# Performance work log

Hardware: AMD Instinct MI355X
Metric: run time of the kernel (lower is better)

The kernel has to match this reference:

```python
import jax, jax.numpy as jnp
import numpy as np

N_NODES = 50000
N_EDGES = 400000
N_GRAPHS = 250
D = 256
NUM_FEATURES = 256
NUM_CLASSES = 10
N_EXTRA_LAYERS = 4  # num_layers - 1
BN_EPS = 1e-5


def _mean_agg(x, src, dst, n):
    # DGL copy_u + mean over incoming edges; zero in-degree nodes get 0.
    s = jax.ops.segment_sum(x[src], dst, num_segments=n)           # [N, d]
    deg = jax.ops.segment_sum(jnp.ones((src.shape[0],), x.dtype), dst, num_segments=n)
    deg = deg[:, None]
    return jnp.where(deg > 0, s / jnp.maximum(deg, 1.0), 0.0)


def _gin_layer(x, src, dst, W1, b1, W2, b2, gamma, beta):
    n = x.shape[0]
    h = x + _mean_agg(x, src, dst, n)                              # (1+eps)*x + agg, eps=0
    h = jax.nn.relu(h @ W1 + b1) @ W2 + b2                         # apply_func MLP
    h = jax.nn.relu(h)                                             # GINConv activation
    mu = h.mean(axis=0)
    var = h.var(axis=0)                                            # biased var (torch BN train)
    return gamma * (h - mu) / jnp.sqrt(var + BN_EPS) + beta


def setup_inputs() -> dict:
    key = jax.random.key(0)
    ks = jax.random.split(key, 24)
    sc_in = 1.0 / np.sqrt(NUM_FEATURES)
    sc = 1.0 / np.sqrt(D)
    inp = {
        "x": jax.random.normal(ks[0], (N_NODES, NUM_FEATURES), dtype=jnp.float32),
        "src": jax.random.randint(ks[1], (N_EDGES,), 0, N_NODES, dtype=jnp.int32),
        "dst": jax.random.randint(ks[2], (N_EDGES,), 0, N_NODES, dtype=jnp.int32),
        "node_counts": jnp.full((N_GRAPHS,), N_NODES // N_GRAPHS, dtype=jnp.int32),
        # conv1 MLP + BN1
        "W1a": jax.random.normal(ks[3], (NUM_FEATURES, D), dtype=jnp.float32) * sc_in,
        "b1a": jnp.zeros((D,), jnp.float32),
        "W1b": jax.random.normal(ks[4], (D, D), dtype=jnp.float32) * sc,
        "b1b": jnp.zeros((D,), jnp.float32),
        "g1": jnp.ones((D,), jnp.float32),
        "be1": jnp.zeros((D,), jnp.float32),
        # stacked convs 2..5 + BNs
        "Ws1": jax.random.normal(ks[5], (N_EXTRA_LAYERS, D, D), dtype=jnp.float32) * sc,
        "bs1": jnp.zeros((N_EXTRA_LAYERS, D), jnp.float32),
        "Ws2": jax.random.normal(ks[6], (N_EXTRA_LAYERS, D, D), dtype=jnp.float32) * sc,
        "bs2": jnp.zeros((N_EXTRA_LAYERS, D), jnp.float32),
        "gammas": jnp.ones((N_EXTRA_LAYERS, D), jnp.float32),
        "betas": jnp.zeros((N_EXTRA_LAYERS, D), jnp.float32),
        # classifier
        "fcW1": jax.random.normal(ks[7], (D, D), dtype=jnp.float32) * sc,
        "fcb1": jnp.zeros((D,), jnp.float32),
        "fcW2": jax.random.normal(ks[8], (D, NUM_CLASSES), dtype=jnp.float32) * sc,
        "fcb2": jnp.zeros((NUM_CLASSES,), jnp.float32),
    }
    return inp


def reference(x, src, dst, node_counts, W1a, b1a, W1b, b1b, g1, be1,
              Ws1, bs1, Ws2, bs2, gammas, betas, fcW1, fcb1, fcW2, fcb2):
    h = _gin_layer(x, src, dst, W1a, b1a, W1b, b1b, g1, be1)
    for i in range(N_EXTRA_LAYERS):
        h = _gin_layer(h, src, dst, Ws1[i], bs1[i], Ws2[i], bs2[i], gammas[i], betas[i])
    # per-graph last-node readout
    last_idx = jnp.cumsum(node_counts) - 1                          # [n_graphs]
    g = h[last_idx]                                                 # [n_graphs, d]
    # dropout is identity in eval mode
    g = jax.nn.relu(g @ fcW1 + fcb1)
    logits = g @ fcW2 + fcb2
    return jax.nn.log_softmax(logits, axis=-1)
```

## Files before the change

kernel.cpp:

```cpp
#include <hip/hip_runtime.h>
#include <hip/hip_bf16.h>

#define N_NODESC 50000
#define N_EDGESC 400000
#define N_GRAPHSC 250
#define DDIM 256
#define NCLS 10
#define BN_EPSF 1e-5f
#define MPAD 50048
#define NBLK_GEMM 391
#define NBLK_SCAN 196

typedef __attribute__((ext_vector_type(4))) float f32x4;
typedef __attribute__((ext_vector_type(8))) short bf16x8;
typedef __attribute__((ext_vector_type(8))) unsigned short u16x8;

__device__ __forceinline__ float bf2f(unsigned short h) {
    union { unsigned int u; float f; } c;
    c.u = ((unsigned int)h) << 16;
    return c.f;
}
__device__ __forceinline__ unsigned short f2bf(float f) {
    union { float f; unsigned int u; } c;
    c.f = f;
    unsigned int u = c.u;
    return (unsigned short)((u + 0x7FFFu + ((u >> 16) & 1u)) >> 16);
}

__device__ __forceinline__ void gld_lds16(const void* g, void* l) {
    __builtin_amdgcn_global_load_lds(
        (const __attribute__((address_space(1))) unsigned int*)g,
        (__attribute__((address_space(3))) unsigned int*)l, 16, 0, 0);
}


__global__ void k_zero32(int* __restrict__ p, int n) {
    int i = blockIdx.x * blockDim.x + threadIdx.x;
    if (i < n) p[i] = 0;
}

__global__ void k_count(const int* __restrict__ dst, int* __restrict__ cnt) {
    int e = blockIdx.x * blockDim.x + threadIdx.x;
    if (e < N_EDGESC) atomicAdd(&cnt[dst[e]], 1);
}

__global__ __launch_bounds__(256) void k_scan1(const int* __restrict__ deg,
                                               int* __restrict__ rowstart,
                                               int* __restrict__ bsum) {
    __shared__ int sh[256];
    int tid = threadIdx.x;
    int i = blockIdx.x * 256 + tid;
    int v = (i < N_NODESC) ? deg[i] : 0;
    sh[tid] = v;
    __syncthreads();
    for (int off = 1; off < 256; off <<= 1) {
        int t = (tid >= off) ? sh[tid - off] : 0;
        __syncthreads();
        sh[tid] += t;
        __syncthreads();
    }
    if (i < N_NODESC) rowstart[i] = sh[tid] - v;
    if (tid == 255) bsum[blockIdx.x] = sh[255];
}

__global__ __launch_bounds__(256) void k_scan2(int* __restrict__ rowstart,
                                               const int* __restrict__ bsum) {
    __shared__ int sh[256];
    int tid = threadIdx.x;
    sh[tid] = (tid < NBLK_SCAN) ? bsum[tid] : 0;
    __syncthreads();
    for (int off = 1; off < 256; off <<= 1) {
        int t = (tid >= off) ? sh[tid - off] : 0;
        __syncthreads();
        sh[tid] += t;
        __syncthreads();
    }
    int i = blockIdx.x * 256 + tid;
    if (blockIdx.x > 0 && i < N_NODESC) rowstart[i] += sh[blockIdx.x - 1];
    if (i == 0) rowstart[N_NODESC] = N_EDGESC;
}

__global__ void k_fill(const int* __restrict__ src, const int* __restrict__ dst,
                       const int* __restrict__ rowstart, int* __restrict__ cur,
                       int* __restrict__ esrc) {
    int e = blockIdx.x * blockDim.x + threadIdx.x;
    if (e < N_EDGESC) {
        int d = dst[e];
        int pos = rowstart[d] + atomicAdd(&cur[d], 1);
        esrc[pos] = src[e];
    }
}


__global__ __launch_bounds__(256) void k_wprep(const float* __restrict__ W1a,
                                               const float* __restrict__ W1b,
                                               const float* __restrict__ Ws1,
                                               const float* __restrict__ Ws2,
                                               unsigned short* __restrict__ Wt) {
    int i = blockIdx.x * blockDim.x + threadIdx.x;
    if (i >= 10 * 65536) return;
    int m = i >> 16;
    int r = i & 65535;
    int n = r >> 8;
    int k = r & 255;
    int l = m >> 1, wsel = m & 1;
    const float* src = (l == 0) ? (wsel ? W1b : W1a)
                                : (wsel ? Ws2 + (size_t)(l - 1) * 65536
                                        : Ws1 + (size_t)(l - 1) * 65536);
    Wt[i] = f2bf(src[(size_t)k * 256 + n]);
}

__global__ __launch_bounds__(256) void k_xbf(const float* __restrict__ X,
                                             unsigned short* __restrict__ Y) {
    int i = blockIdx.x * 256 + threadIdx.x;
    if (i < N_NODESC * 64) {
        float4 v = ((const float4*)X)[i];
        ushort4 o;
        o.x = f2bf(v.x); o.y = f2bf(v.y); o.z = f2bf(v.z); o.w = f2bf(v.w);
        ((ushort4*)Y)[i] = o;
    }
}


__global__ __launch_bounds__(256) void k_agg_bf(const unsigned short* __restrict__ X,
                                                const int* __restrict__ esrc,
                                                const int* __restrict__ rowstart,
                                                const float* __restrict__ stat,
                                                const float* __restrict__ gamma,
                                                const float* __restrict__ beta,
                                                unsigned short* __restrict__ Hout) {
    int node = blockIdx.x * 8 + (threadIdx.x >> 5);
    if (node >= N_NODESC) return;
    int lane = threadIdx.x & 31;
    int d0 = lane * 8;
    float sc[8], tt[8];
    if (stat) {
        const float invN = 1.0f / (float)N_NODESC;
#pragma unroll
        for (int q = 0; q < 8; q++) {
            float mu = stat[d0 + q] * invN;
            float var = stat[256 + d0 + q] * invN - mu * mu;
            float s = gamma[d0 + q] * rsqrtf(var + BN_EPSF);
            sc[q] = s;
            tt[q] = beta[d0 + q] - s * mu;
        }
    } else {
#pragma unroll
        for (int q = 0; q < 8; q++) { sc[q] = 1.f; tt[q] = 0.f; }
    }
    int beg = rowstart[node];
    int end = rowstart[node + 1];
    float s0[8], s1[8], s2[8], s3[8];
#pragma unroll
    for (int q = 0; q < 8; q++) { s0[q] = 0.f; s1[q] = 0.f; s2[q] = 0.f; s3[q] = 0.f; }
    int j = beg;
    for (; j + 4 <= end; j += 4) {
        int sn0 = esrc[j], sn1 = esrc[j + 1], sn2 = esrc[j + 2], sn3 = esrc[j + 3];
        u16x8 v0 = *(const u16x8*)(X + (size_t)sn0 * DDIM + d0);
        u16x8 v1 = *(const u16x8*)(X + (size_t)sn1 * DDIM + d0);
        u16x8 v2 = *(const u16x8*)(X + (size_t)sn2 * DDIM + d0);
        u16x8 v3 = *(const u16x8*)(X + (size_t)sn3 * DDIM + d0);
#pragma unroll
        for (int q = 0; q < 8; q++) {
            s0[q] += bf2f(v0[q]);
            s1[q] += bf2f(v1[q]);
            s2[q] += bf2f(v2[q]);
            s3[q] += bf2f(v3[q]);
        }
    }
    for (; j < end; j++) {
        int sn0 = esrc[j];
        u16x8 v0 = *(const u16x8*)(X + (size_t)sn0 * DDIM + d0);
#pragma unroll
        for (int q = 0; q < 8; q++) s0[q] += bf2f(v0[q]);
    }
    float inv = (end > beg) ? 1.0f / (float)(end - beg) : 0.0f;
    float cnt = (end > beg) ? 2.0f : 1.0f;
    u16x8 xv = *(const u16x8*)(X + (size_t)node * DDIM + d0);
    u16x8 o;
#pragma unroll
    for (int q = 0; q < 8; q++) {
        float s = s0[q] + s1[q] + s2[q] + s3[q];
        o[q] = f2bf(sc[q] * (bf2f(xv[q]) + s * inv) + tt[q] * cnt);
    }
    *(u16x8*)(Hout + (size_t)node * DDIM + d0) = o;
}


__global__ __launch_bounds__(256) void k_gemm(const unsigned short* __restrict__ A,
                                              const unsigned short* __restrict__ Wt,
                                              const float* __restrict__ bias,
                                              unsigned short* __restrict__ C,
                                              float* __restrict__ part) {
    __shared__ unsigned short As[128 * 64];
    __shared__ unsigned short Bs[128 * 64];
    __shared__ unsigned short Ct[128 * 128];
    __shared__ float sred[2][256];

    const int tid = threadIdx.x;
    const int wv = tid >> 6;
    const int lane = tid & 63;
    const int bm = blockIdx.x;
    const int bn = blockIdx.y;

    const int wr = (wv >> 1) * 64;
    const int wc = (wv & 1) * 64;
    const int lr = lane & 15;
    const int lk = lane >> 4;

    f32x4 acc[4][4];
#pragma unroll
    for (int m = 0; m < 4; m++)
#pragma unroll
        for (int n = 0; n < 4; n++) acc[m][n] = (f32x4)(0.f);

    for (int k0 = 0; k0 < 256; k0 += 64) {
#pragma unroll
        for (int i = 0; i < 4; i++) {
            int c = wv * 256 + i * 64 + lane;
            int row = c >> 3;
            int kc = (c & 7) ^ (row & 7);
            gld_lds16(A + (size_t)(bm * 128 + row) * 256 + k0 + kc * 8,
                      (void*)&As[(size_t)c * 8]);
            gld_lds16(Wt + (size_t)(bn * 128 + row) * 256 + k0 + kc * 8,
                      (void*)&Bs[(size_t)c * 8]);
        }
        __syncthreads();

#pragma unroll
        for (int ks = 0; ks < 2; ks++) {
            bf16x8 af[4], bfr[4];
#pragma unroll
            for (int m = 0; m < 4; m++) {
                int row = wr + m * 16 + lr;
                af[m] = ((const bf16x8*)As)[row * 8 + ((ks * 4 + lk) ^ (row & 7))];
            }
#pragma unroll
            for (int n = 0; n < 4; n++) {
                int row = wc + n * 16 + lr;
                bfr[n] = ((const bf16x8*)Bs)[row * 8 + ((ks * 4 + lk) ^ (row & 7))];
            }
#pragma unroll
            for (int m = 0; m < 4; m++)
#pragma unroll
                for (int n = 0; n < 4; n++)
                    acc[m][n] = __builtin_amdgcn_mfma_f32_16x16x32_bf16(
                        af[m], bfr[n], acc[m][n], 0, 0, 0);
        }
        __syncthreads();
    }

#pragma unroll
    for (int n = 0; n < 4; n++) {
        int cloc = wc + n * 16 + lr;
        float bv = bias[bn * 128 + cloc];
        float sp = 0.f, ssp = 0.f;
#pragma unroll
        for (int m = 0; m < 4; m++)
#pragma unroll
            for (int i = 0; i < 4; i++) {
                int row = wr + m * 16 + lk * 4 + i;
                float v = fmaxf(acc[m][n][i] + bv, 0.f);
                Ct[row * 128 + (((cloc >> 3) ^ (row & 7)) << 3) + (cloc & 7)] = f2bf(v);
                if (bm * 128 + row < N_NODESC) { sp += v; ssp += v * v; }
            }
        if (part) {
            sp += __shfl_xor(sp, 16);
            sp += __shfl_xor(sp, 32);
            ssp += __shfl_xor(ssp, 16);
            ssp += __shfl_xor(ssp, 32);
            if (lane < 16) {
                sred[wv >> 1][cloc] = sp;
                sred[wv >> 1][128 + cloc] = ssp;
            }
        }
    }
    __syncthreads();

#pragma unroll
    for (int it = 0; it < 8; it++) {
        int chunk = it * 256 + tid;
        int row = chunk >> 4;
        int cc = chunk & 15;
        u16x8 v = *(const u16x8*)&Ct[row * 128 + ((cc ^ (row & 7)) << 3)];
        *(u16x8*)(C + (size_t)(bm * 128 + row) * DDIM + bn * 128 + cc * 8) = v;
    }
    if (part && tid < 256) {
        float v = sred[0][tid] + sred[1][tid];
        int cloc = tid & 127;
        int off = (tid < 128) ? (bn * 128 + cloc) : (256 + bn * 128 + cloc);
        part[(size_t)bm * 512 + off] = v;
    }
}


__global__ __launch_bounds__(512) void k_statred1(const float* __restrict__ part,
                                                  float* __restrict__ part2) {
    int t = threadIdx.x;
    int b0 = blockIdx.x * 17;
    float s = 0.f;
#pragma unroll 4
    for (int j = 0; j < 17; j++) s += part[(size_t)(b0 + j) * 512 + t];
    part2[(size_t)blockIdx.x * 512 + t] = s;
}

__global__ __launch_bounds__(512) void k_statred2(const float* __restrict__ part2,
                                                  float* __restrict__ stat) {
    int t = threadIdx.x;
    float s = 0.f;
#pragma unroll 4
    for (int j = 0; j < 23; j++) s += part2[(size_t)j * 512 + t];
    stat[t] = s;
}


__global__ __launch_bounds__(256) void k_head(const unsigned short* __restrict__ Y,
                                              const int* __restrict__ counts,
                                              const float* __restrict__ stat,
                                              const float* __restrict__ gamma,
                                              const float* __restrict__ beta,
                                              const float* __restrict__ fcW1,
                                              const float* __restrict__ fcb1,
                                              const float* __restrict__ fcW2,
                                              const float* __restrict__ fcb2,
                                              float* __restrict__ out) {
    int g = blockIdx.x;
    __shared__ float row[DDIM];
    __shared__ float gv[DDIM];
    __shared__ float logits[NCLS];
    __shared__ int lastIdx;
    if (threadIdx.x == 0) {
        int s = 0;
        for (int i = 0; i <= g; i++) s += counts[i];
        lastIdx = s - 1;
    }
    __syncthreads();
    int j = threadIdx.x;
    const float invN = 1.0f / (float)N_NODESC;
    float mu = stat[j] * invN;
    float var = stat[256 + j] * invN - mu * mu;
    float sc = gamma[j] * rsqrtf(var + BN_EPSF);
    row[j] = sc * (bf2f(Y[(size_t)lastIdx * DDIM + j]) - mu) + beta[j];
    __syncthreads();
    float acc = fcb1[j];
    for (int d = 0; d < DDIM; d++) acc += row[d] * fcW1[(size_t)d * DDIM + j];
    gv[j] = fmaxf(acc, 0.f);
    __syncthreads();
    if (j < NCLS) {
        float a = fcb2[j];
        for (int d = 0; d < DDIM; d++) a += gv[d] * fcW2[(size_t)d * NCLS + j];
        logits[j] = a;
    }
    __syncthreads();
    if (j == 0) {
        float m = -1e30f;
        for (int c = 0; c < NCLS; c++) m = fmaxf(m, logits[c]);
        float se = 0.f;
        for (int c = 0; c < NCLS; c++) se += expf(logits[c] - m);
        float lse = m + logf(se);
        for (int c = 0; c < NCLS; c++) out[g * NCLS + c] = logits[c] - lse;
    }
}


extern "C" void kernel_launch(void* const* d_in, const int* in_sizes, int n_in,
                              void* d_out, int out_size, void* d_ws, size_t ws_size,
                              hipStream_t stream) {
    const float* x    = (const float*)d_in[0];
    const int* src    = (const int*)d_in[1];
    const int* dst    = (const int*)d_in[2];
    const int* counts = (const int*)d_in[3];
    const float* W1a  = (const float*)d_in[4];
    const float* b1a  = (const float*)d_in[5];
    const float* W1b  = (const float*)d_in[6];
    const float* b1b  = (const float*)d_in[7];
    const float* g1   = (const float*)d_in[8];
    const float* be1  = (const float*)d_in[9];
    const float* Ws1  = (const float*)d_in[10];
    const float* bs1  = (const float*)d_in[11];
    const float* Ws2  = (const float*)d_in[12];
    const float* bs2  = (const float*)d_in[13];
    const float* gms  = (const float*)d_in[14];
    const float* bts  = (const float*)d_in[15];
    const float* fcW1 = (const float*)d_in[16];
    const float* fcb1 = (const float*)d_in[17];
    const float* fcW2 = (const float*)d_in[18];
    const float* fcb2 = (const float*)d_in[19];
    float* out = (float*)d_out;

    char* ws = (char*)d_ws;
    const size_t BUF = (size_t)MPAD * DDIM * 2;
    unsigned short* B0 = (unsigned short*)(ws);
    unsigned short* B1 = (unsigned short*)(ws + BUF);
    unsigned short* B2 = (unsigned short*)(ws + 2 * BUF);
    unsigned short* Bx = (unsigned short*)(ws + 3 * BUF);
    unsigned short* Wt = (unsigned short*)(ws + 4 * BUF);
    int* rowstart      = (int*)(ws + 4 * BUF + 1310720);
    int* cursor        = (int*)(ws + 4 * BUF + 1510784);
    int* esrc          = (int*)(ws + 4 * BUF + 1710848);
    float* stats       = (float*)(ws + 4 * BUF + 3310848);
    int* bsum          = (int*)(ws + 4 * BUF + 3321088);
    float* stats_part  = (float*)(ws + 4 * BUF + 3321872 + 16);
    float* stats_part2 = (float*)(ws + 4 * BUF + 4122656 + 32);

    k_zero32<<<dim3((N_NODESC + 255) / 256), 256, 0, stream>>>(cursor, N_NODESC);
    k_count<<<dim3((N_EDGESC + 255) / 256), 256, 0, stream>>>(dst, cursor);
    k_scan1<<<dim3(NBLK_SCAN), 256, 0, stream>>>(cursor, rowstart, bsum);
    k_scan2<<<dim3(NBLK_SCAN), 256, 0, stream>>>(rowstart, bsum);
    k_zero32<<<dim3((N_NODESC + 255) / 256), 256, 0, stream>>>(cursor, N_NODESC);
    k_fill<<<dim3((N_EDGESC + 255) / 256), 256, 0, stream>>>(src, dst, rowstart,
                                                             cursor, esrc);

    k_wprep<<<dim3((10 * 65536 + 255) / 256), 256, 0, stream>>>(W1a, W1b, Ws1, Ws2, Wt);
    k_xbf<<<dim3(12500), 256, 0, stream>>>(x, Bx);

    for (int l = 0; l < 5; ++l) {
        const float* B1b = (l == 0) ? b1a : bs1 + (l - 1) * 256;
        const float* B2b = (l == 0) ? b1b : bs2 + (l - 1) * 256;
        const unsigned short* Wt1 = Wt + (size_t)(l * 2) * 65536;
        const unsigned short* Wt2 = Wt + (size_t)(l * 2 + 1) * 65536;

        if (l == 0) {
            k_agg_bf<<<dim3(6250), 256, 0, stream>>>(Bx, esrc, rowstart, nullptr,
                                                     nullptr, nullptr, B1);
        } else {
            const float* GA = (l == 1) ? g1 : gms + (l - 2) * 256;
            const float* BE = (l == 1) ? be1 : bts + (l - 2) * 256;
            k_agg_bf<<<dim3(6250), 256, 0, stream>>>(B0, esrc, rowstart,
                                                     stats + (size_t)(l - 1) * 512,
                                                     GA, BE, B1);
        }
        k_gemm<<<dim3(NBLK_GEMM, 2), 256, 0, stream>>>(B1, Wt1, B1b, B2, nullptr);
        k_gemm<<<dim3(NBLK_GEMM, 2), 256, 0, stream>>>(B2, Wt2, B2b, B0, stats_part);
        k_statred1<<<dim3(23), 512, 0, stream>>>(stats_part, stats_part2);
        k_statred2<<<dim3(1), 512, 0, stream>>>(stats_part2,
                                                stats + (size_t)l * 512);
    }

    k_head<<<dim3(N_GRAPHSC), 256, 0, stream>>>(B0, counts, stats + 4 * 512,
                                                gms + 3 * 256, bts + 3 * 256,
                                                fcW1, fcb1, fcW2, fcb2, out);
}
```

Baseline: 520.3 us.

## Sort nodes by in-degree for aggregation and fuse BN stat reduction via atomics

Adds a degree histogram, scan and scatter that build a node order sorted by in-degree (descending), and the aggregation kernel now processes nodes in that order. Warps in the same block then see similar edge counts, which reduces load imbalance. The two-stage BN statistics reduction kernels are removed, and the second GEMM atomically adds its per-block partial sums straight into the stats buffer, which is zeroed by an enlarged initial zero kernel. The cost is a few extra preprocessing launches, less locality in node writes, and float atomics whose summation order is nondeterministic.

```diff
diff --git a/kernel.cpp b/kernel.cpp
--- a/kernel.cpp
+++ b/kernel.cpp
@@ -42,6 +42,33 @@
 __global__ void k_count(const int* __restrict__ dst, int* __restrict__ cnt) {
     int e = blockIdx.x * blockDim.x + threadIdx.x;
     if (e < N_EDGESC) atomicAdd(&cnt[dst[e]], 1);
+}
+
+__global__ void k_dhist(const int* __restrict__ deg, int* __restrict__ dhist) {
+    int i = blockIdx.x * blockDim.x + threadIdx.x;
+    if (i < N_NODESC) atomicAdd(&dhist[min(deg[i], 63)], 1);
+}
+
+__global__ void k_dscan(const int* __restrict__ dhist, int* __restrict__ dbase) {
+    __shared__ int sh[64];
+    int t = threadIdx.x;
+    sh[t] = dhist[t];
+    __syncthreads();
+    int s = 0;
+    for (int b = t + 1; b < 64; b++) s += sh[b];
+    dbase[t] = s;
+}
+
+__global__ void k_dscatter(const int* __restrict__ rowstart,
+                           const int* __restrict__ dbase, int* __restrict__ dcur,
+                           int* __restrict__ order) {
+    int i = blockIdx.x * blockDim.x + threadIdx.x;
+    if (i < N_NODESC) {
+        int deg = rowstart[i + 1] - rowstart[i];
+        int bin = min(deg, 63);
+        int pos = dbase[bin] + atomicAdd(&dcur[bin], 1);
+        order[pos] = i;
+    }
 }
 
 __global__ __launch_bounds__(256) void k_scan1(const int* __restrict__ deg,
@@ -125,12 +152,14 @@
 __global__ __launch_bounds__(256) void k_agg_bf(const unsigned short* __restrict__ X,
                                                 const int* __restrict__ esrc,
                                                 const int* __restrict__ rowstart,
+                                                const int* __restrict__ order,
                                                 const float* __restrict__ stat,
                                                 const float* __restrict__ gamma,
                                                 const float* __restrict__ beta,
                                                 unsigned short* __restrict__ Hout) {
-    int node = blockIdx.x * 8 + (threadIdx.x >> 5);
-    if (node >= N_NODESC) return;
+    int slot = blockIdx.x * 8 + (threadIdx.x >> 5);
+    if (slot >= N_NODESC) return;
+    int node = order[slot];
     int lane = threadIdx.x & 31;
     int d0 = lane * 8;
     float sc[8], tt[8];
@@ -191,7 +220,7 @@
                                               const unsigned short* __restrict__ Wt,
                                               const float* __restrict__ bias,
                                               unsigned short* __restrict__ C,
-                                              float* __restrict__ part) {
+                                              float* __restrict__ statg) {
     __shared__ unsigned short As[128 * 64];
     __shared__ unsigned short Bs[128 * 64];
     __shared__ unsigned short Ct[128 * 128];
@@ -264,7 +293,7 @@
                 Ct[row * 128 + (((cloc >> 3) ^ (row & 7)) << 3) + (cloc & 7)] = f2bf(v);
                 if (bm * 128 + row < N_NODESC) { sp += v; ssp += v * v; }
             }
-        if (part) {
+        if (statg) {
             sp += __shfl_xor(sp, 16);
             sp += __shfl_xor(sp, 32);
             ssp += __shfl_xor(ssp, 16);
@@ -285,32 +314,12 @@
         u16x8 v = *(const u16x8*)&Ct[row * 128 + ((cc ^ (row & 7)) << 3)];
         *(u16x8*)(C + (size_t)(bm * 128 + row) * DDIM + bn * 128 + cc * 8) = v;
     }
-    if (part && tid < 256) {
+    if (statg && tid < 256) {
         float v = sred[0][tid] + sred[1][tid];
         int cloc = tid & 127;
         int off = (tid < 128) ? (bn * 128 + cloc) : (256 + bn * 128 + cloc);
-        part[(size_t)bm * 512 + off] = v;
-    }
-}
-
-
-__global__ __launch_bounds__(512) void k_statred1(const float* __restrict__ part,
-                                                  float* __restrict__ part2) {
-    int t = threadIdx.x;
-    int b0 = blockIdx.x * 17;
-    float s = 0.f;
-#pragma unroll 4
-    for (int j = 0; j < 17; j++) s += part[(size_t)(b0 + j) * 512 + t];
-    part2[(size_t)blockIdx.x * 512 + t] = s;
-}
-
-__global__ __launch_bounds__(512) void k_statred2(const float* __restrict__ part2,
-                                                  float* __restrict__ stat) {
-    int t = threadIdx.x;
-    float s = 0.f;
-#pragma unroll 4
-    for (int j = 0; j < 23; j++) s += part2[(size_t)j * 512 + t];
-    stat[t] = s;
+        atomicAdd(&statg[off], v);
+    }
 }
 
 
@@ -394,22 +403,29 @@
     unsigned short* B1 = (unsigned short*)(ws + BUF);
     unsigned short* B2 = (unsigned short*)(ws + 2 * BUF);
     unsigned short* Bx = (unsigned short*)(ws + 3 * BUF);
-    unsigned short* Wt = (unsigned short*)(ws + 4 * BUF);
-    int* rowstart      = (int*)(ws + 4 * BUF + 1310720);
-    int* cursor        = (int*)(ws + 4 * BUF + 1510784);
-    int* esrc          = (int*)(ws + 4 * BUF + 1710848);
-    float* stats       = (float*)(ws + 4 * BUF + 3310848);
-    int* bsum          = (int*)(ws + 4 * BUF + 3321088);
-    float* stats_part  = (float*)(ws + 4 * BUF + 3321872 + 16);
-    float* stats_part2 = (float*)(ws + 4 * BUF + 4122656 + 32);
-
-    k_zero32<<<dim3((N_NODESC + 255) / 256), 256, 0, stream>>>(cursor, N_NODESC);
+    char* base4 = ws + 4 * BUF;
+    unsigned short* Wt = (unsigned short*)(base4);
+    int* rowstart      = (int*)(base4 + 1310720);
+    int* cursor        = (int*)(base4 + 1510784);
+    int* dhist         = (int*)(base4 + 1710848);
+    int* dcur          = (int*)(base4 + 1711104);
+    float* stats       = (float*)(base4 + 1711360);
+    int* dbase         = (int*)(base4 + 1721600);
+    int* esrc          = (int*)(base4 + 1721856);
+    int* order         = (int*)(base4 + 3321856);
+    int* bsum          = (int*)(base4 + 3522048);
+
+    k_zero32<<<dim3(206), 256, 0, stream>>>(cursor, 52704);
+
     k_count<<<dim3((N_EDGESC + 255) / 256), 256, 0, stream>>>(dst, cursor);
+    k_dhist<<<dim3(NBLK_SCAN), 256, 0, stream>>>(cursor, dhist);
     k_scan1<<<dim3(NBLK_SCAN), 256, 0, stream>>>(cursor, rowstart, bsum);
     k_scan2<<<dim3(NBLK_SCAN), 256, 0, stream>>>(rowstart, bsum);
+    k_dscan<<<dim3(1), 64, 0, stream>>>(dhist, dbase);
     k_zero32<<<dim3((N_NODESC + 255) / 256), 256, 0, stream>>>(cursor, N_NODESC);
     k_fill<<<dim3((N_EDGESC + 255) / 256), 256, 0, stream>>>(src, dst, rowstart,
                                                              cursor, esrc);
+    k_dscatter<<<dim3(NBLK_SCAN), 256, 0, stream>>>(rowstart, dbase, dcur, order);
 
     k_wprep<<<dim3((10 * 65536 + 255) / 256), 256, 0, stream>>>(W1a, W1b, Ws1, Ws2, Wt);
     k_xbf<<<dim3(12500), 256, 0, stream>>>(x, Bx);
@@ -421,20 +437,18 @@
         const unsigned short* Wt2 = Wt + (size_t)(l * 2 + 1) * 65536;
 
         if (l == 0) {
-            k_agg_bf<<<dim3(6250), 256, 0, stream>>>(Bx, esrc, rowstart, nullptr,
-                                                     nullptr, nullptr, B1);
+            k_agg_bf<<<dim3(6250), 256, 0, stream>>>(Bx, esrc, rowstart, order,
+                                                     nullptr, nullptr, nullptr, B1);
         } else {
             const float* GA = (l == 1) ? g1 : gms + (l - 2) * 256;
             const float* BE = (l == 1) ? be1 : bts + (l - 2) * 256;
-            k_agg_bf<<<dim3(6250), 256, 0, stream>>>(B0, esrc, rowstart,
+            k_agg_bf<<<dim3(6250), 256, 0, stream>>>(B0, esrc, rowstart, order,
                                                      stats + (size_t)(l - 1) * 512,
                                                      GA, BE, B1);
         }
         k_gemm<<<dim3(NBLK_GEMM, 2), 256, 0, stream>>>(B1, Wt1, B1b, B2, nullptr);
-        k_gemm<<<dim3(NBLK_GEMM, 2), 256, 0, stream>>>(B2, Wt2, B2b, B0, stats_part);
-        k_statred1<<<dim3(23), 512, 0, stream>>>(stats_part, stats_part2);
-        k_statred2<<<dim3(1), 512, 0, stream>>>(stats_part2,
-                                                stats + (size_t)l * 512);
+        k_gemm<<<dim3(NBLK_GEMM, 2), 256, 0, stream>>>(B2, Wt2, B2b, B0,
+                                                       stats + (size_t)l * 512);
     }
 
     k_head<<<dim3(N_GRAPHSC), 256, 0, stream>>>(B0, counts, stats + 4 * 512,
```

Result: slower. 870.9 us (+67.4%).
